# Performance work log

Measured on AMD Instinct MI355X. Metric: run time of the kernel, lower is better.

Reference implementation:

```python
import jax, jax.numpy as jnp
import numpy as np

N_NODES = 10000
N_EDGES = 320000
K_HOPS = 3
IN_CH = 128
OUT_CH = 128


def setup_inputs() -> dict:
    key = jax.random.key(0)
    k1, k2, k3, k4, k5 = jax.random.split(key, 5)
    h = jax.random.normal(k1, (N_NODES, IN_CH), dtype=jnp.float32)
    X = jax.random.normal(k2, (N_EDGES, K_HOPS), dtype=jnp.float32)
    edge_index = jax.random.randint(k3, (2, N_EDGES), 0, N_NODES, dtype=jnp.int64)
    batch_node = jax.random.uniform(k4, (N_NODES,), dtype=jnp.float32)
    # glorot init for weight, zeros for bias (matches reset_parameters)
    stdv = np.sqrt(6.0 / (IN_CH + OUT_CH))
    weight = jax.random.uniform(k5, (K_HOPS, IN_CH, OUT_CH), dtype=jnp.float32,
                                minval=-stdv, maxval=stdv)
    bias = jnp.zeros((OUT_CH,), dtype=jnp.float32)
    return {"h": h, "X": X, "edge_index": edge_index,
            "batch_node": batch_node, "weight": weight, "bias": bias}


def reference(h, X, edge_index, batch_node, weight, bias):
    # Original builds dense A[k, src, dst] = X[e, k] (zeros elsewhere), then
    # res = A @ h @ weight, max over k, + bias. We honor the sparsity:
    # agg[src, k, :] = sum_e X[e, k] * h[dst[e], :]  (sparse A @ h per hop k)
    n = batch_node.shape[0]
    src = edge_index[0]
    dst = edge_index[1]
    msg = X[:, :, None] * h[dst][:, None, :]                 # [E, K, in]
    agg = jax.ops.segment_sum(msg, src, num_segments=n)      # [N, K, in]
    res = jnp.einsum('nki,kio->kno', agg, weight)            # [K, N, out]
    out = res.max(axis=0) + bias                             # [N, out]
    return out
```

## Files before the change

### kernel.cpp

```cpp
#include <hip/hip_runtime.h>

#define N_NODES 10000
#define N_EDGES 320000
#define K_HOPS  3
#define CH      128
#define NBF     16
#define ROWP    136
#define SUBSLOT 44
#define SLOT    88
#define SEPAD   96
#define CSTRIDE 16

#define EDGE_BLKS 1250
#define HCV_BLKS  1250
#define WCV_BLKS  192

typedef __attribute__((ext_vector_type(8))) short  frag8;
typedef __attribute__((ext_vector_type(4))) float  floatx4;

__device__ inline unsigned short f2bf(float x) {
    union { float f; unsigned u; } v; v.f = x;
    unsigned r = v.u + 0x7fff + ((v.u >> 16) & 1);
    return (unsigned short)(r >> 16);
}

__global__ __launch_bounds__(256) void prep_fill_kernel(
    const float* __restrict__ h, const float* __restrict__ X,
    const int* __restrict__ ei, const float* __restrict__ W,
    unsigned short* __restrict__ hb, unsigned short* __restrict__ WT,
    int* __restrict__ cursor, uint2* __restrict__ edata)
{
    int b = blockIdx.x;
    if (b < EDGE_BLKS) {
        int e = b * 256 + threadIdx.x;
        int src = ei[e];
        int dst = ei[N_EDGES + e];
        int j = e & 1;
        int r = atomicAdd(cursor + (2 * src + j) * CSTRIDE, 1);
        if (r < SUBSLOT) {
            uint2 rec;
            rec.x = (unsigned)f2bf(X[e * K_HOPS + 0])
                  | ((unsigned)f2bf(X[e * K_HOPS + 1]) << 16);
            rec.y = (unsigned)f2bf(X[e * K_HOPS + 2])
                  | ((unsigned)dst << 16);
            edata[(size_t)src * SLOT + j * SUBSLOT + r] = rec;
        }
    } else if (b < EDGE_BLKS + HCV_BLKS) {
        int tid = (b - EDGE_BLKS) * 256 + threadIdx.x;
        float4 v = *(const float4*)(h + (size_t)tid * 4);
        ushort4 p;
        p.x = f2bf(v.x); p.y = f2bf(v.y); p.z = f2bf(v.z); p.w = f2bf(v.w);
        *(ushort4*)(hb + (size_t)tid * 4) = p;
    } else {
        int tid = (b - EDGE_BLKS - HCV_BLKS) * 256 + threadIdx.x;
        int i = tid & 127;
        int o = (tid >> 7) & 127;
        int k = tid >> 14;
        WT[tid] = f2bf(W[((size_t)k * CH + i) * CH + o]);
    }
}

__device__ inline void estep(uint2 er, uint2 q, float (&a)[12]) {
    float x0 = __uint_as_float(er.x << 16);
    float x1 = __uint_as_float(er.x & 0xffff0000u);
    float x2 = __uint_as_float(er.y << 16);
    float h0 = __uint_as_float(q.x << 16);
    float h1 = __uint_as_float(q.x & 0xffff0000u);
    float h2 = __uint_as_float(q.y << 16);
    float h3 = __uint_as_float(q.y & 0xffff0000u);
    a[0] = fmaf(x0, h0, a[0]); a[1]  = fmaf(x0, h1, a[1]);
    a[2] = fmaf(x0, h2, a[2]); a[3]  = fmaf(x0, h3, a[3]);
    a[4] = fmaf(x1, h0, a[4]); a[5]  = fmaf(x1, h1, a[5]);
    a[6] = fmaf(x1, h2, a[6]); a[7]  = fmaf(x1, h3, a[7]);
    a[8] = fmaf(x2, h0, a[8]); a[9]  = fmaf(x2, h1, a[9]);
    a[10]= fmaf(x2, h2, a[10]); a[11]= fmaf(x2, h3, a[11]);
}

__global__ __launch_bounds__(512) void fused_kernel(
    const unsigned short* __restrict__ hb,
    const uint2*          __restrict__ edata,
    const int*            __restrict__ cursor,
    const unsigned short* __restrict__ WT,
    const float*          __restrict__ bias,
    float*                __restrict__ out)
{
    __shared__ unsigned short sA[K_HOPS][16][ROWP];
    __shared__ uint2 sE[NBF][SEPAD];
    const int node0 = blockIdx.x * NBF;
    const int t    = threadIdx.x;
    const int w    = t >> 6;
    const int lane = t & 63;
    const int half = lane >> 5;
    const int cq   = (lane & 31) * 4;

    const int rA = 2 * w, rB = rA + 1;
    const int nA = node0 + rA, nB = node0 + rB;
    int a0 = __builtin_amdgcn_readfirstlane(min(cursor[(2 * nA + 0) * CSTRIDE], SUBSLOT));
    int a1 = __builtin_amdgcn_readfirstlane(min(cursor[(2 * nA + 1) * CSTRIDE], SUBSLOT));
    int b0 = __builtin_amdgcn_readfirstlane(min(cursor[(2 * nB + 0) * CSTRIDE], SUBSLOT));
    int b1 = __builtin_amdgcn_readfirstlane(min(cursor[(2 * nB + 1) * CSTRIDE], SUBSLOT));
    const int cA = a0 + a1, cB = b0 + b1;
    const uint2* eA = edata + (size_t)nA * SLOT;
    const uint2* eB = edata + (size_t)nB * SLOT;

    if (lane < a0) sE[rA][lane]      = eA[lane];
    if (lane < a1) sE[rA][a0 + lane] = eA[SUBSLOT + lane];
    if (lane < b0) sE[rB][lane]      = eB[lane];
    if (lane < b1) sE[rB][b0 + lane] = eB[SUBSLOT + lane];
    {
        uint2 zz; zz.x = 0u; zz.y = 0u;
        int zA0 = cA + lane, zA1 = cA + 64 + lane;
        if (zA0 < SEPAD) sE[rA][zA0] = zz;
        if (zA1 < SEPAD) sE[rA][zA1] = zz;
        int zB0 = cB + lane, zB1 = cB + 64 + lane;
        if (zB0 < SEPAD) sE[rB][zB0] = zz;
        if (zB1 < SEPAD) sE[rB][zB1] = zz;
    }

    float accA[12], accB[12];
#pragma unroll
    for (int i = 0; i < 12; ++i) { accA[i] = 0.f; accB[i] = 0.f; }

    const int gmax = (max(cA, cB) + 15) >> 4;
    for (int g = 0; g < gmax; ++g) {
        const int s = g * 8;
        uint2 erA[8], erB[8], qA[8], qB[8];
#pragma unroll
        for (int k = 0; k < 8; ++k) erA[k] = sE[rA][2 * (s + k) + half];
#pragma unroll
        for (int k = 0; k < 8; ++k) erB[k] = sE[rB][2 * (s + k) + half];
#pragma unroll
        for (int k = 0; k < 8; ++k)
            qA[k] = *(const uint2*)(hb + ((size_t)(erA[k].y >> 16) << 7) + cq);
#pragma unroll
        for (int k = 0; k < 8; ++k)
            qB[k] = *(const uint2*)(hb + ((size_t)(erB[k].y >> 16) << 7) + cq);
#pragma unroll
        for (int k = 0; k < 8; ++k) estep(erA[k], qA[k], accA);
#pragma unroll
        for (int k = 0; k < 8; ++k) estep(erB[k], qB[k], accB);
    }

#pragma unroll
    for (int i = 0; i < 12; ++i) {
        accA[i] += __shfl_xor(accA[i], 32, 64);
        accB[i] += __shfl_xor(accB[i], 32, 64);
    }

    if (half == 0) {
#pragma unroll
        for (int hop = 0; hop < K_HOPS; ++hop) {
            ushort4 pA, pB;
            pA.x = f2bf(accA[4 * hop + 0]); pA.y = f2bf(accA[4 * hop + 1]);
            pA.z = f2bf(accA[4 * hop + 2]); pA.w = f2bf(accA[4 * hop + 3]);
            pB.x = f2bf(accB[4 * hop + 0]); pB.y = f2bf(accB[4 * hop + 1]);
            pB.z = f2bf(accB[4 * hop + 2]); pB.w = f2bf(accB[4 * hop + 3]);
            *(ushort4*)&sA[hop][rA][cq] = pA;
            *(ushort4*)&sA[hop][rB][cq] = pB;
        }
    }
    __syncthreads();

    const int col  = lane & 15;
    const int quad = lane >> 4;
    const int ob   = 16 * w;

    floatx4 m0 = {-3.4e38f, -3.4e38f, -3.4e38f, -3.4e38f};
#pragma unroll
    for (int hop = 0; hop < K_HOPS; ++hop) {
        floatx4 cv = {0.f, 0.f, 0.f, 0.f};
        const unsigned short* arow = &sA[hop][col][quad * 8];
        const unsigned short* bp   = WT + ((size_t)hop * CH + ob + col) * CH + quad * 8;
#pragma unroll
        for (int kt = 0; kt < 4; ++kt) {
            frag8 af = *(const frag8*)(arow + kt * 32);
            frag8 bf = *(const frag8*)(bp + kt * 32);
            cv = __builtin_amdgcn_mfma_f32_16x16x32_bf16(af, bf, cv, 0, 0, 0);
        }
#pragma unroll
        for (int r = 0; r < 4; ++r) m0[r] = fmaxf(m0[r], cv[r]);
    }

    const float bv = bias[ob + col];
#pragma unroll
    for (int r = 0; r < 4; ++r) {
        int row = quad * 4 + r;
        out[(size_t)(node0 + row) * CH + ob + col] = m0[r] + bv;
    }
}

extern "C" void kernel_launch(void* const* d_in, const int* in_sizes, int n_in,
                              void* d_out, int out_size, void* d_ws, size_t ws_size,
                              hipStream_t stream) {
    const float* h    = (const float*)d_in[0];
    const float* X    = (const float*)d_in[1];
    const int*   ei   = (const int*)  d_in[2];
    const float* W    = (const float*)d_in[4];
    const float* bias = (const float*)d_in[5];
    float*       out  = (float*)d_out;

    char* ws = (char*)d_ws;
    int* cursor = (int*)ws;                        ws += (size_t)N_NODES * 2 * CSTRIDE * sizeof(int);
    unsigned short* hb = (unsigned short*)ws;      ws += (size_t)N_NODES * CH * sizeof(unsigned short);
    unsigned short* WT = (unsigned short*)ws;      ws += (size_t)K_HOPS * CH * CH * sizeof(unsigned short);
    uint2* edata = (uint2*)ws;

    hipMemsetAsync(cursor, 0, (size_t)N_NODES * 2 * CSTRIDE * sizeof(int), stream);

    prep_fill_kernel<<<EDGE_BLKS + HCV_BLKS + WCV_BLKS, 256, 0, stream>>>(
        h, X, ei, W, hb, WT, cursor, edata);
    fused_kernel<<<(N_NODES + NBF - 1) / NBF, 512, 0, stream>>>(
        hb, edata, cursor, WT, bias, out);
}
```

Baseline: 111.1 us.

## Gather neighbor rows with 16-byte loads and shrink blocks to eight nodes

The aggregation loop now has 16 lanes cover a 128-channel bf16 row with uint4 loads, so each wave instruction gathers four edges. Accumulators double per thread, and partial sums are reduced with two cross-lane shuffles instead of one. Blocks shrink to 8 nodes and 256 threads, with an occupancy hint, and each wave computes 32 output columns through two MFMA chains that share A fragments. The intent is fewer, wider gather transactions and more resident blocks. In exchange, half of each 16-row MFMA tile now holds unused rows, and weight reads from global memory double across the grid.

```diff
diff --git a/kernel.cpp b/kernel.cpp
--- a/kernel.cpp
+++ b/kernel.cpp
@@ -4,7 +4,7 @@
 #define N_EDGES 320000
 #define K_HOPS  3
 #define CH      128
-#define NBF     16
+#define NBF     8
 #define ROWP    136
 #define SUBSLOT 44
 #define SLOT    88
@@ -22,6 +22,11 @@
     union { float f; unsigned u; } v; v.f = x;
     unsigned r = v.u + 0x7fff + ((v.u >> 16) & 1);
     return (unsigned short)(r >> 16);
+}
+__device__ inline float bflo(unsigned u) { return __uint_as_float(u << 16); }
+__device__ inline float bfhi(unsigned u) { return __uint_as_float(u & 0xffff0000u); }
+__device__ inline unsigned pk2(float a, float b) {
+    return (unsigned)f2bf(a) | ((unsigned)f2bf(b) << 16);
 }
 
 __global__ __launch_bounds__(256) void prep_fill_kernel(
@@ -60,23 +65,19 @@
     }
 }
 
-__device__ inline void estep(uint2 er, uint2 q, float (&a)[12]) {
-    float x0 = __uint_as_float(er.x << 16);
-    float x1 = __uint_as_float(er.x & 0xffff0000u);
-    float x2 = __uint_as_float(er.y << 16);
-    float h0 = __uint_as_float(q.x << 16);
-    float h1 = __uint_as_float(q.x & 0xffff0000u);
-    float h2 = __uint_as_float(q.y << 16);
-    float h3 = __uint_as_float(q.y & 0xffff0000u);
-    a[0] = fmaf(x0, h0, a[0]); a[1]  = fmaf(x0, h1, a[1]);
-    a[2] = fmaf(x0, h2, a[2]); a[3]  = fmaf(x0, h3, a[3]);
-    a[4] = fmaf(x1, h0, a[4]); a[5]  = fmaf(x1, h1, a[5]);
-    a[6] = fmaf(x1, h2, a[6]); a[7]  = fmaf(x1, h3, a[7]);
-    a[8] = fmaf(x2, h0, a[8]); a[9]  = fmaf(x2, h1, a[9]);
-    a[10]= fmaf(x2, h2, a[10]); a[11]= fmaf(x2, h3, a[11]);
-}
-
-__global__ __launch_bounds__(512) void fused_kernel(
+__device__ inline void estep4(uint2 er, uint4 q, float (&a)[24]) {
+    float x0 = bflo(er.x), x1 = bfhi(er.x), x2 = bflo(er.y);
+    float hh[8] = { bflo(q.x), bfhi(q.x), bflo(q.y), bfhi(q.y),
+                    bflo(q.z), bfhi(q.z), bflo(q.w), bfhi(q.w) };
+#pragma unroll
+    for (int c = 0; c < 8; ++c) {
+        a[c]      = fmaf(x0, hh[c], a[c]);
+        a[8 + c]  = fmaf(x1, hh[c], a[8 + c]);
+        a[16 + c] = fmaf(x2, hh[c], a[16 + c]);
+    }
+}
+
+__global__ __launch_bounds__(256, 5) void fused_kernel(
     const unsigned short* __restrict__ hb,
     const uint2*          __restrict__ edata,
     const int*            __restrict__ cursor,
@@ -90,8 +91,8 @@
     const int t    = threadIdx.x;
     const int w    = t >> 6;
     const int lane = t & 63;
-    const int half = lane >> 5;
-    const int cq   = (lane & 31) * 4;
+    const int quad = lane >> 4;
+    const int cl   = (lane & 15) * 8;
 
     const int rA = 2 * w, rB = rA + 1;
     const int nA = node0 + rA, nB = node0 + rB;
@@ -117,75 +118,95 @@
         if (zB1 < SEPAD) sE[rB][zB1] = zz;
     }
 
-    float accA[12], accB[12];
-#pragma unroll
-    for (int i = 0; i < 12; ++i) { accA[i] = 0.f; accB[i] = 0.f; }
-
-    const int gmax = (max(cA, cB) + 15) >> 4;
+    float accA[24], accB[24];
+#pragma unroll
+    for (int i = 0; i < 24; ++i) { accA[i] = 0.f; accB[i] = 0.f; }
+
+    const int gmax = (max(cA, cB) + 7) >> 3;
     for (int g = 0; g < gmax; ++g) {
         const int s = g * 8;
-        uint2 erA[8], erB[8], qA[8], qB[8];
-#pragma unroll
-        for (int k = 0; k < 8; ++k) erA[k] = sE[rA][2 * (s + k) + half];
-#pragma unroll
-        for (int k = 0; k < 8; ++k) erB[k] = sE[rB][2 * (s + k) + half];
-#pragma unroll
-        for (int k = 0; k < 8; ++k)
-            qA[k] = *(const uint2*)(hb + ((size_t)(erA[k].y >> 16) << 7) + cq);
-#pragma unroll
-        for (int k = 0; k < 8; ++k)
-            qB[k] = *(const uint2*)(hb + ((size_t)(erB[k].y >> 16) << 7) + cq);
-#pragma unroll
-        for (int k = 0; k < 8; ++k) estep(erA[k], qA[k], accA);
-#pragma unroll
-        for (int k = 0; k < 8; ++k) estep(erB[k], qB[k], accB);
-    }
-
-#pragma unroll
-    for (int i = 0; i < 12; ++i) {
+        uint2 eA0 = sE[rA][s + quad];
+        uint2 eA1 = sE[rA][s + 4 + quad];
+        uint2 eB0 = sE[rB][s + quad];
+        uint2 eB1 = sE[rB][s + 4 + quad];
+        uint4 qA0 = *(const uint4*)(hb + ((size_t)(eA0.y >> 16) << 7) + cl);
+        uint4 qA1 = *(const uint4*)(hb + ((size_t)(eA1.y >> 16) << 7) + cl);
+        uint4 qB0 = *(const uint4*)(hb + ((size_t)(eB0.y >> 16) << 7) + cl);
+        uint4 qB1 = *(const uint4*)(hb + ((size_t)(eB1.y >> 16) << 7) + cl);
+        estep4(eA0, qA0, accA);
+        estep4(eA1, qA1, accA);
+        estep4(eB0, qB0, accB);
+        estep4(eB1, qB1, accB);
+    }
+
+#pragma unroll
+    for (int i = 0; i < 24; ++i) {
+        accA[i] += __shfl_xor(accA[i], 16, 64);
         accA[i] += __shfl_xor(accA[i], 32, 64);
+        accB[i] += __shfl_xor(accB[i], 16, 64);
         accB[i] += __shfl_xor(accB[i], 32, 64);
     }
 
-    if (half == 0) {
+    if (quad == 0) {
 #pragma unroll
         for (int hop = 0; hop < K_HOPS; ++hop) {
-            ushort4 pA, pB;
-            pA.x = f2bf(accA[4 * hop + 0]); pA.y = f2bf(accA[4 * hop + 1]);
-            pA.z = f2bf(accA[4 * hop + 2]); pA.w = f2bf(accA[4 * hop + 3]);
-            pB.x = f2bf(accB[4 * hop + 0]); pB.y = f2bf(accB[4 * hop + 1]);
-            pB.z = f2bf(accB[4 * hop + 2]); pB.w = f2bf(accB[4 * hop + 3]);
-            *(ushort4*)&sA[hop][rA][cq] = pA;
-            *(ushort4*)&sA[hop][rB][cq] = pB;
+            uint4 vA, vB;
+            vA.x = pk2(accA[8 * hop + 0], accA[8 * hop + 1]);
+            vA.y = pk2(accA[8 * hop + 2], accA[8 * hop + 3]);
+            vA.z = pk2(accA[8 * hop + 4], accA[8 * hop + 5]);
+            vA.w = pk2(accA[8 * hop + 6], accA[8 * hop + 7]);
+            vB.x = pk2(accB[8 * hop + 0], accB[8 * hop + 1]);
+            vB.y = pk2(accB[8 * hop + 2], accB[8 * hop + 3]);
+            vB.z = pk2(accB[8 * hop + 4], accB[8 * hop + 5]);
+            vB.w = pk2(accB[8 * hop + 6], accB[8 * hop + 7]);
+            *(uint4*)&sA[hop][rA][cl] = vA;
+            *(uint4*)&sA[hop][rB][cl] = vB;
         }
     }
     __syncthreads();
 
-    const int col  = lane & 15;
-    const int quad = lane >> 4;
-    const int ob   = 16 * w;
-
-    floatx4 m0 = {-3.4e38f, -3.4e38f, -3.4e38f, -3.4e38f};
+    const int col = lane & 15;
+    const int ob0 = 32 * w, ob1 = ob0 + 16;
+
+    floatx4 m0a = {-3.4e38f, -3.4e38f, -3.4e38f, -3.4e38f};
+    floatx4 m0b = {-3.4e38f, -3.4e38f, -3.4e38f, -3.4e38f};
 #pragma unroll
     for (int hop = 0; hop < K_HOPS; ++hop) {
-        floatx4 cv = {0.f, 0.f, 0.f, 0.f};
+        frag8 af[4];
         const unsigned short* arow = &sA[hop][col][quad * 8];
-        const unsigned short* bp   = WT + ((size_t)hop * CH + ob + col) * CH + quad * 8;
+#pragma unroll
+        for (int kt = 0; kt < 4; ++kt) af[kt] = *(const frag8*)(arow + kt * 32);
+
+        const unsigned short* bp0 = WT + ((size_t)hop * CH + ob0 + col) * CH + quad * 8;
+        floatx4 cv0 = {0.f, 0.f, 0.f, 0.f};
 #pragma unroll
         for (int kt = 0; kt < 4; ++kt) {
-            frag8 af = *(const frag8*)(arow + kt * 32);
-            frag8 bf = *(const frag8*)(bp + kt * 32);
-            cv = __builtin_amdgcn_mfma_f32_16x16x32_bf16(af, bf, cv, 0, 0, 0);
-        }
-#pragma unroll
-        for (int r = 0; r < 4; ++r) m0[r] = fmaxf(m0[r], cv[r]);
-    }
-
-    const float bv = bias[ob + col];
-#pragma unroll
-    for (int r = 0; r < 4; ++r) {
-        int row = quad * 4 + r;
-        out[(size_t)(node0 + row) * CH + ob + col] = m0[r] + bv;
+            frag8 bf = *(const frag8*)(bp0 + kt * 32);
+            cv0 = __builtin_amdgcn_mfma_f32_16x16x32_bf16(af[kt], bf, cv0, 0, 0, 0);
+        }
+#pragma unroll
+        for (int r = 0; r < 4; ++r) m0a[r] = fmaxf(m0a[r], cv0[r]);
+
+        const unsigned short* bp1 = WT + ((size_t)hop * CH + ob1 + col) * CH + quad * 8;
+        floatx4 cv1 = {0.f, 0.f, 0.f, 0.f};
+#pragma unroll
+        for (int kt = 0; kt < 4; ++kt) {
+            frag8 bf = *(const frag8*)(bp1 + kt * 32);
+            cv1 = __builtin_amdgcn_mfma_f32_16x16x32_bf16(af[kt], bf, cv1, 0, 0, 0);
+        }
+#pragma unroll
+        for (int r = 0; r < 4; ++r) m0b[r] = fmaxf(m0b[r], cv1[r]);
+    }
+
+    if (quad < 2) {
+        const float bv0 = bias[ob0 + col];
+        const float bv1 = bias[ob1 + col];
+#pragma unroll
+        for (int r = 0; r < 4; ++r) {
+            int row = quad * 4 + r;
+            out[(size_t)(node0 + row) * CH + ob0 + col] = m0a[r] + bv0;
+            out[(size_t)(node0 + row) * CH + ob1 + col] = m0b[r] + bv1;
+        }
     }
 }
 
@@ -209,6 +230,6 @@
 
     prep_fill_kernel<<<EDGE_BLKS + HCV_BLKS + WCV_BLKS, 256, 0, stream>>>(
         h, X, ei, W, hb, WT, cursor, edata);
-    fused_kernel<<<(N_NODES + NBF - 1) / NBF, 512, 0, stream>>>(
+    fused_kernel<<<(N_NODES + NBF - 1) / NBF, 256, 0, stream>>>(
         hb, edata, cursor, WT, bias, out);
 }
```

Result: slower. 120.6 us (+8.5%).
